# Optimization experiments

Hardware: AMD Instinct MI355X
Metric: run time of the kernel (lower is better)

The kernel has to match this reference:

```python
import jax, jax.numpy as jnp
import numpy as np

L, H, P = 16384, 512, 512
DT_MIN, DT_MAX = 1e-3, 1e-1


def setup_inputs() -> dict:
    key = jax.random.key(0)
    ks = jax.random.split(key, 9)
    u = jax.random.normal(ks[0], (L, H), dtype=jnp.float32)
    # stable diagonal state matrix: Re(Lambda) < 0 (HiPPO-style init)
    Lambda_re = -(0.5 * jax.random.uniform(ks[1], (P,), dtype=jnp.float32) + 1e-3)
    Lambda_im = jnp.pi * jax.random.normal(ks[2], (P,), dtype=jnp.float32)
    # lecun-normal-ish scaling for B (fan-in H) and C (fan-in P)
    B_re = jax.random.normal(ks[3], (P, H), dtype=jnp.float32) / jnp.sqrt(2.0 * H)
    B_im = jax.random.normal(ks[4], (P, H), dtype=jnp.float32) / jnp.sqrt(2.0 * H)
    C_re = jax.random.normal(ks[5], (H, P), dtype=jnp.float32) / jnp.sqrt(2.0 * P)
    C_im = jax.random.normal(ks[6], (H, P), dtype=jnp.float32) / jnp.sqrt(2.0 * P)
    D = jax.random.uniform(ks[7], (H,), dtype=jnp.float32)
    # init_log_steps: uniform in [log(dt_min), log(dt_max)]
    lo, hi = np.log(DT_MIN), np.log(DT_MAX)
    log_step = jax.random.uniform(ks[8], (P,), dtype=jnp.float32, minval=lo, maxval=hi)
    return {"u": u, "Lambda_re": Lambda_re, "Lambda_im": Lambda_im,
            "B_re": B_re, "B_im": B_im, "C_re": C_re, "C_im": C_im,
            "D": D, "log_step": log_step}


def _binary_op(q_i, q_j):
    # associative combine for diagonal linear recurrence (elementwise over (L, P))
    A_i, b_i = q_i
    A_j, b_j = q_j
    return (A_j * A_i, A_j * b_i + b_j)


def reference(u, Lambda_re, Lambda_im, B_re, B_im, C_re, C_im, D, log_step):
    Lambda = Lambda_re + 1j * Lambda_im            # (P,) complex64
    B_tilde = B_re + 1j * B_im                     # (P, H)
    C_tilde = C_re + 1j * C_im                     # (H, P)
    step = jnp.exp(log_step)                       # (P,)
    # zero-order-hold discretization
    Lambda_bar = jnp.exp(Lambda * step)            # (P,)
    B_bar = ((Lambda_bar - 1.0) / Lambda)[:, None] * B_tilde  # (P, H)
    # Bu_t = B_bar @ u_t for all t, as one GEMM: (L, H) @ (H, P)
    Bu = u.astype(B_bar.dtype) @ B_bar.T           # (L, P) complex
    Lambda_el = jnp.broadcast_to(Lambda_bar, Bu.shape)  # (L, P)
    _, xs = jax.lax.associative_scan(_binary_op, (Lambda_el, Bu))  # xs: (L, P)
    # y_t = Re(C_tilde @ x_t) + D * u_t, batched as one GEMM
    ys = (xs @ C_tilde.T).real + D * u             # (L, H)
    return ys.astype(jnp.float32)
```

## Files before the change

### kernel.cpp

```cpp
#include <hip/hip_runtime.h>
#include <stdint.h>

#define L_DIM 16384
#define H_DIM 512
#define P_DIM 512
#define T_CH  32
#define NC    (L_DIM / T_CH)
#define LP    ((size_t)L_DIM * P_DIM)
#define LH    ((size_t)L_DIM * H_DIM)

typedef unsigned short u16;
typedef __attribute__((ext_vector_type(8))) _Float16 f16x8;
typedef __attribute__((ext_vector_type(4))) float f32x4;
typedef __attribute__((ext_vector_type(8))) unsigned short u16x8;

__device__ __forceinline__ u16 f2h(float x) {
    _Float16 h = (_Float16)x;
    return __builtin_bit_cast(u16, h);
}
__device__ __forceinline__ float h2f(u16 h) {
    return (float)__builtin_bit_cast(_Float16, h);
}

__device__ __forceinline__ void gload16(const void* g, void* lds) {
    __builtin_amdgcn_global_load_lds(
        (const __attribute__((address_space(1))) void*)g,
        (__attribute__((address_space(3))) void*)(uintptr_t)lds,
        16, 0, 0);
}

__device__ __forceinline__ f32x4 mfma_f16(f16x8 a, f16x8 b, f32x4 c) {
    return __builtin_amdgcn_mfma_f32_16x16x32_f16(a, b, c, 0, 0, 0);
}

__global__ __launch_bounds__(P_DIM) void prep_kernel(
    const float* __restrict__ Lre, const float* __restrict__ Lim,
    const float* __restrict__ log_step,
    float* __restrict__ lbr, float* __restrict__ lbi,
    float* __restrict__ gre, float* __restrict__ gim,
    float* __restrict__ powr, float* __restrict__ powi)
{
    int p = threadIdx.x;
    float st = expf(log_step[p]);
    float ar = Lre[p] * st, ai = Lim[p] * st;
    float er = expf(ar);
    float lr = er * cosf(ai), li = er * sinf(ai);
    lbr[p] = lr; lbi[p] = li;
    float den = Lre[p] * Lre[p] + Lim[p] * Lim[p];
    float x = lr - 1.0f, y = li;
    gre[p] = (x * Lre[p] + y * Lim[p]) / den;
    gim[p] = (y * Lre[p] - x * Lim[p]) / den;
    float pr = 1.f, pi2 = 0.f;
    powr[p] = 1.f; powi[p] = 0.f;
    for (int k = 1; k <= T_CH; ++k) {
        float nr = pr * lr - pi2 * li;
        float ni = pr * li + pi2 * lr;
        pr = nr; pi2 = ni;
        powr[(size_t)k * P_DIM + p] = pr;
        powi[(size_t)k * P_DIM + p] = pi2;
    }
}

__global__ __launch_bounds__(256) void convert_u(
    const float* __restrict__ u, u16* __restrict__ uh)
{
    size_t i = ((size_t)blockIdx.x * 256 + threadIdx.x) * 8;
    float4 v0 = *(const float4*)(u + i);
    float4 v1 = *(const float4*)(u + i + 4);
    u16x8 h;
    h[0] = f2h(v0.x); h[1] = f2h(v0.y); h[2] = f2h(v0.z); h[3] = f2h(v0.w);
    h[4] = f2h(v1.x); h[5] = f2h(v1.y); h[6] = f2h(v1.z); h[7] = f2h(v1.w);
    *(u16x8*)(uh + i) = h;
}

__global__ __launch_bounds__(256) void build_bcat(
    const float* __restrict__ Bre, const float* __restrict__ Bim,
    const float* __restrict__ gre, const float* __restrict__ gim,
    u16* __restrict__ Bcat)
{
    int idx = blockIdx.x * 256 + threadIdx.x;
    int p = idx >> 9, h = idx & 511;
    float br = Bre[idx], bi = Bim[idx];
    float gr = gre[p], gi = gim[p];
    Bcat[(size_t)p * 512 + h]         = f2h(gr * br - gi * bi);
    Bcat[(size_t)(512 + p) * 512 + h] = f2h(gr * bi + gi * br);
}

__global__ __launch_bounds__(256) void build_ccat(
    const float* __restrict__ Cre, const float* __restrict__ Cim,
    u16* __restrict__ Ccat)
{
    int idx = blockIdx.x * 256 + threadIdx.x;
    int h = idx >> 9, p = idx & 511;
    size_t row = (size_t)h * 1024;
    Ccat[row + p]       = f2h(Cre[idx]);
    Ccat[row + 512 + p] = f2h(-Cim[idx]);
}

template<int KTOT, int NBN, int MODE>
__global__ __launch_bounds__(256, 2) void gemm_mfma(
    const u16* __restrict__ A0, const u16* __restrict__ A1,
    const u16* __restrict__ Bmat,
    void* __restrict__ O0v, void* __restrict__ O1v,
    const float* __restrict__ Dvec, const u16* __restrict__ uIn,
    const float* __restrict__ powr, const float* __restrict__ powi,
    float* __restrict__ Rwr, float* __restrict__ Rwi,
    float* __restrict__ Iwr, float* __restrict__ Iwi)
{
    __shared__ u16 Als[128 * 64];
    __shared__ u16 Bls[128 * 64];

    const u16* Aseg[2] = {A0, A1};

    int b = blockIdx.x;
    int m = (b & 7) * 16 + b / (8 * NBN);
    int n = (b >> 3) & (NBN - 1);
    int m0 = m * 128, n0 = n * 128;

    int tid = threadIdx.x;
    int w = tid >> 6, lane = tid & 63;
    int wm = w >> 1, wn = w & 1;

    f32x4 acc[4][4];
    #pragma unroll
    for (int i = 0; i < 4; ++i)
        #pragma unroll
        for (int j = 0; j < 4; ++j) acc[i][j] = (f32x4)0.f;

    int lr8  = lane >> 3;
    int slin = lane & 7;

    char* AlsB = (char*)&Als[0];
    char* BlsB = (char*)&Bls[0];

    const int NSEG = KTOT / 512;
    #pragma unroll
    for (int seg = 0; seg < NSEG; ++seg) {
        const u16* Ap = Aseg[seg];
        for (int k8 = 0; k8 < 8; ++k8) {
            int ko = k8 * 64;
            int kB = seg * 512 + ko;

            __syncthreads();
            #pragma unroll
            for (int c = 0; c < 4; ++c) {
                int sidx = w * 4 + c;
                int r = sidx * 8 + lr8;
                int g = slin ^ (r & 7);
                const u16* ga = Ap + (size_t)(m0 + r) * 512 + ko + g * 8;
                gload16(ga, AlsB + sidx * 1024);
                const u16* gb = Bmat + (size_t)(n0 + r) * KTOT + kB + g * 8;
                gload16(gb, BlsB + sidx * 1024);
            }
            asm volatile("s_waitcnt vmcnt(0)" ::: "memory");
            __syncthreads();

            f16x8 a[4][2], bf[4][2];
            #pragma unroll
            for (int mm = 0; mm < 4; ++mm)
                #pragma unroll
                for (int kk = 0; kk < 2; ++kk) {
                    int row = wm * 64 + mm * 16 + (lane & 15);
                    int sl  = kk * 4 + (lane >> 4);
                    int off = row * 128 + ((sl ^ (lane & 7)) << 4);
                    a[mm][kk] = *(const f16x8*)(AlsB + off);
                }
            #pragma unroll
            for (int nn = 0; nn < 4; ++nn)
                #pragma unroll
                for (int kk = 0; kk < 2; ++kk) {
                    int row = wn * 64 + nn * 16 + (lane & 15);
                    int sl  = kk * 4 + (lane >> 4);
                    int off = row * 128 + ((sl ^ (lane & 7)) << 4);
                    bf[nn][kk] = *(const f16x8*)(BlsB + off);
                }
            #pragma unroll
            for (int mm = 0; mm < 4; ++mm)
                #pragma unroll
                for (int nn = 0; nn < 4; ++nn) {
                    acc[mm][nn] = mfma_f16(a[mm][0], bf[nn][0], acc[mm][nn]);
                    acc[mm][nn] = mfma_f16(a[mm][1], bf[nn][1], acc[mm][nn]);
                }
        }
    }

    int colb = n0 + wn * 64;
    int rowb = m0 + wm * 64;
    #pragma unroll
    for (int mm = 0; mm < 4; ++mm)
        #pragma unroll
        for (int nn = 0; nn < 4; ++nn) {
            f32x4 v = acc[mm][nn];
            int col = colb + nn * 16 + (lane & 15);
            #pragma unroll
            for (int j = 0; j < 4; ++j) {
                int row = rowb + mm * 16 + (lane >> 4) * 4 + j;
                if constexpr (MODE == 0) {
                    size_t oidx = (size_t)row * 512 + (col & 511);
                    u16 hv = f2h(v[j]);
                    if (col < 512) ((u16*)O0v)[oidx] = hv;
                    else           ((u16*)O1v)[oidx] = hv;
                } else {
                    size_t oidx = (size_t)row * 512 + col;
                    ((float*)O0v)[oidx] = v[j] + Dvec[col] * h2f(uIn[oidx]);
                }
            }
        }

    if constexpr (MODE == 0) {
        float swr[2][4] = {{0.f}};
        float swi[2][4] = {{0.f}};
        #pragma unroll
        for (int mm = 0; mm < 4; ++mm) {
            int ch = mm >> 1;
            #pragma unroll
            for (int nn = 0; nn < 4; ++nn) {
                int col = colb + nn * 16 + (lane & 15);
                int p = col & 511;
                f32x4 v = acc[mm][nn];
                #pragma unroll
                for (int j = 0; j < 4; ++j) {
                    int k = (mm & 1) * 16 + (lane >> 4) * 4 + j;
                    int e = (T_CH - 1) - k;
                    float wr = powr[(size_t)e * 512 + p];
                    float wi = powi[(size_t)e * 512 + p];
                    swr[ch][nn] = fmaf(wr, v[j], swr[ch][nn]);
                    swi[ch][nn] = fmaf(wi, v[j], swi[ch][nn]);
                }
            }
        }
        #pragma unroll
        for (int ch = 0; ch < 2; ++ch)
            #pragma unroll
            for (int nn = 0; nn < 4; ++nn) {
                float a2 = swr[ch][nn];
                a2 += __shfl_xor(a2, 16); a2 += __shfl_xor(a2, 32);
                swr[ch][nn] = a2;
                float b2 = swi[ch][nn];
                b2 += __shfl_xor(b2, 16); b2 += __shfl_xor(b2, 32);
                swi[ch][nn] = b2;
            }
        if (lane < 16) {
            #pragma unroll
            for (int ch = 0; ch < 2; ++ch) {
                int c = (m0 >> 5) + wm * 2 + ch;
                #pragma unroll
                for (int nn = 0; nn < 4; ++nn) {
                    int col = colb + nn * 16 + lane;
                    int p = col & 511;
                    size_t pidx = (size_t)c * 512 + p;
                    if (col < 512) { Rwr[pidx] = swr[ch][nn]; Rwi[pidx] = swi[ch][nn]; }
                    else           { Iwr[pidx] = swr[ch][nn]; Iwi[pidx] = swi[ch][nn]; }
                }
            }
        }
    }
}

__global__ __launch_bounds__(64) void scan_chunks(
    const float* __restrict__ Rwr, const float* __restrict__ Rwi,
    const float* __restrict__ Iwr, const float* __restrict__ Iwi,
    const float* __restrict__ powr, const float* __restrict__ powi,
    float* __restrict__ carr, float* __restrict__ cari)
{
    int p = blockIdx.x * 64 + threadIdx.x;
    float ar = powr[(size_t)T_CH * P_DIM + p];
    float ai = powi[(size_t)T_CH * P_DIM + p];
    float sr = 0.f, si = 0.f;
    #pragma unroll 8
    for (int c = 0; c < NC; ++c) {
        size_t idx = (size_t)c * P_DIM + p;
        carr[idx] = sr; cari[idx] = si;
        float vre = Rwr[idx] - Iwi[idx];
        float vim = Rwi[idx] + Iwr[idx];
        float nr = fmaf(ar, sr, fmaf(-ai, si, vre));
        float ni = fmaf(ar, si, fmaf( ai, sr, vim));
        sr = nr; si = ni;
    }
}

__global__ __launch_bounds__(P_DIM) void scan_fix(
    const u16* __restrict__ burh, const u16* __restrict__ buih,
    const float* __restrict__ lbr, const float* __restrict__ lbi,
    const float* __restrict__ carr, const float* __restrict__ cari,
    u16* __restrict__ xrh, u16* __restrict__ xih)
{
    int p = threadIdx.x;
    int c = blockIdx.x;
    float lr = lbr[p], li = lbi[p];
    float xr = carr[(size_t)c * P_DIM + p];
    float xi = cari[(size_t)c * P_DIM + p];
    size_t base = (size_t)c * T_CH * P_DIM + p;
    #pragma unroll 4
    for (int k = 0; k < T_CH; ++k) {
        size_t idx = base + (size_t)k * P_DIM;
        float br = h2f(burh[idx]), bi = h2f(buih[idx]);
        float nr = fmaf(lr, xr, fmaf(-li, xi, br));
        float ni = fmaf(lr, xi, fmaf( li, xr, bi));
        xr = nr; xi = ni;
        xrh[idx] = f2h(xr);
        xih[idx] = f2h(xi);
    }
}

extern "C" void kernel_launch(void* const* d_in, const int* in_sizes, int n_in,
                              void* d_out, int out_size, void* d_ws, size_t ws_size,
                              hipStream_t stream)
{
    const float* u        = (const float*)d_in[0];
    const float* Lre      = (const float*)d_in[1];
    const float* Lim      = (const float*)d_in[2];
    const float* Bre      = (const float*)d_in[3];
    const float* Bim      = (const float*)d_in[4];
    const float* Cre      = (const float*)d_in[5];
    const float* Cim      = (const float*)d_in[6];
    const float* D        = (const float*)d_in[7];
    const float* log_step = (const float*)d_in[8];
    float* out = (float*)d_out;

    char* w8 = (char*)d_ws;
    u16*   burh = (u16*)(w8);
    u16*   buih = (u16*)(w8 + 16777216);
    u16*   xrh  = (u16*)(w8 + 33554432);
    u16*   xih  = (u16*)(w8 + 50331648);
    u16*   uh   = (u16*)(w8 + 67108864);
    u16*   Bcat = (u16*)(w8 + 83886080);
    u16*   Ccat = (u16*)(w8 + 84934656);
    float* Rwr  = (float*)(w8 + 85983232);
    float* Rwi  = (float*)(w8 + 87031808);
    float* Iwr  = (float*)(w8 + 88080384);
    float* Iwi  = (float*)(w8 + 89128960);
    float* carr = (float*)(w8 + 90177536);
    float* cari = (float*)(w8 + 91226112);
    float* powr = (float*)(w8 + 92274688);
    float* powi = (float*)(w8 + 92342272);
    float* lbr  = (float*)(w8 + 92409856);
    float* lbi  = lbr + P_DIM;
    float* gre  = lbi + P_DIM;
    float* gim  = gre + P_DIM;

    prep_kernel<<<1, P_DIM, 0, stream>>>(Lre, Lim, log_step, lbr, lbi, gre, gim, powr, powi);
    convert_u<<<(int)(LH / 2048), 256, 0, stream>>>(u, uh);
    build_bcat<<<(P_DIM * H_DIM) / 256, 256, 0, stream>>>(Bre, Bim, gre, gim, Bcat);
    build_ccat<<<(H_DIM * P_DIM) / 256, 256, 0, stream>>>(Cre, Cim, Ccat);

    gemm_mfma<512, 8, 0><<<1024, 256, 0, stream>>>(
        uh, uh, Bcat, burh, buih, nullptr, nullptr,
        powr, powi, Rwr, Rwi, Iwr, Iwi);

    scan_chunks<<<8, 64, 0, stream>>>(Rwr, Rwi, Iwr, Iwi, powr, powi, carr, cari);
    scan_fix<<<NC, P_DIM, 0, stream>>>(burh, buih, lbr, lbi, carr, cari, xrh, xih);

    gemm_mfma<1024, 4, 1><<<512, 256, 0, stream>>>(
        xrh, xih, Ccat, out, nullptr, D, uh,
        nullptr, nullptr, nullptr, nullptr, nullptr, nullptr);
}
```

Baseline: 130.6 us.

## Fuse prep, conversion, and B/C build kernels into one front kernel

Merges the four small setup kernels (lambda discretisation and powers, u-to-half conversion, B and C concatenation) into a single launch that partitions blocks by role. The B build now recomputes the ZOH gain per element instead of reading it from a buffer written by a serialized one-block prep kernel. This removes launch overhead and the dependency chain between prep and B build. It also reorders the chunk-weight reduction in the first GEMM epilogue so each power value loaded is reused for both chunk halves.

```diff
diff --git a/kernel.cpp b/kernel.cpp
--- a/kernel.cpp
+++ b/kernel.cpp
@@ -33,68 +33,72 @@
     return __builtin_amdgcn_mfma_f32_16x16x32_f16(a, b, c, 0, 0, 0);
 }
 
-__global__ __launch_bounds__(P_DIM) void prep_kernel(
-    const float* __restrict__ Lre, const float* __restrict__ Lim,
-    const float* __restrict__ log_step,
-    float* __restrict__ lbr, float* __restrict__ lbi,
-    float* __restrict__ gre, float* __restrict__ gim,
-    float* __restrict__ powr, float* __restrict__ powi)
-{
-    int p = threadIdx.x;
+__device__ __forceinline__ void zoh_lambda(
+    const float* Lre, const float* Lim, const float* log_step, int p,
+    float& lr, float& li)
+{
     float st = expf(log_step[p]);
     float ar = Lre[p] * st, ai = Lim[p] * st;
     float er = expf(ar);
-    float lr = er * cosf(ai), li = er * sinf(ai);
-    lbr[p] = lr; lbi[p] = li;
-    float den = Lre[p] * Lre[p] + Lim[p] * Lim[p];
-    float x = lr - 1.0f, y = li;
-    gre[p] = (x * Lre[p] + y * Lim[p]) / den;
-    gim[p] = (y * Lre[p] - x * Lim[p]) / den;
-    float pr = 1.f, pi2 = 0.f;
-    powr[p] = 1.f; powi[p] = 0.f;
-    for (int k = 1; k <= T_CH; ++k) {
-        float nr = pr * lr - pi2 * li;
-        float ni = pr * li + pi2 * lr;
-        pr = nr; pi2 = ni;
-        powr[(size_t)k * P_DIM + p] = pr;
-        powi[(size_t)k * P_DIM + p] = pi2;
-    }
-}
-
-__global__ __launch_bounds__(256) void convert_u(
-    const float* __restrict__ u, u16* __restrict__ uh)
-{
-    size_t i = ((size_t)blockIdx.x * 256 + threadIdx.x) * 8;
-    float4 v0 = *(const float4*)(u + i);
-    float4 v1 = *(const float4*)(u + i + 4);
-    u16x8 h;
-    h[0] = f2h(v0.x); h[1] = f2h(v0.y); h[2] = f2h(v0.z); h[3] = f2h(v0.w);
-    h[4] = f2h(v1.x); h[5] = f2h(v1.y); h[6] = f2h(v1.z); h[7] = f2h(v1.w);
-    *(u16x8*)(uh + i) = h;
-}
-
-__global__ __launch_bounds__(256) void build_bcat(
+    lr = er * cosf(ai);
+    li = er * sinf(ai);
+}
+
+__global__ __launch_bounds__(256) void front_kernel(
+    const float* __restrict__ u,
+    const float* __restrict__ Lre, const float* __restrict__ Lim,
+    const float* __restrict__ log_step,
     const float* __restrict__ Bre, const float* __restrict__ Bim,
-    const float* __restrict__ gre, const float* __restrict__ gim,
-    u16* __restrict__ Bcat)
-{
-    int idx = blockIdx.x * 256 + threadIdx.x;
-    int p = idx >> 9, h = idx & 511;
-    float br = Bre[idx], bi = Bim[idx];
-    float gr = gre[p], gi = gim[p];
-    Bcat[(size_t)p * 512 + h]         = f2h(gr * br - gi * bi);
-    Bcat[(size_t)(512 + p) * 512 + h] = f2h(gr * bi + gi * br);
-}
-
-__global__ __launch_bounds__(256) void build_ccat(
     const float* __restrict__ Cre, const float* __restrict__ Cim,
-    u16* __restrict__ Ccat)
-{
-    int idx = blockIdx.x * 256 + threadIdx.x;
-    int h = idx >> 9, p = idx & 511;
-    size_t row = (size_t)h * 1024;
-    Ccat[row + p]       = f2h(Cre[idx]);
-    Ccat[row + 512 + p] = f2h(-Cim[idx]);
+    u16* __restrict__ uh, u16* __restrict__ Bcat, u16* __restrict__ Ccat,
+    float* __restrict__ lbr, float* __restrict__ lbi,
+    float* __restrict__ powr, float* __restrict__ powi)
+{
+    int b = blockIdx.x;
+    if (b < 4096) {
+        size_t i = ((size_t)b * 256 + threadIdx.x) * 8;
+        float4 v0 = *(const float4*)(u + i);
+        float4 v1 = *(const float4*)(u + i + 4);
+        u16x8 h;
+        h[0] = f2h(v0.x); h[1] = f2h(v0.y); h[2] = f2h(v0.z); h[3] = f2h(v0.w);
+        h[4] = f2h(v1.x); h[5] = f2h(v1.y); h[6] = f2h(v1.z); h[7] = f2h(v1.w);
+        *(u16x8*)(uh + i) = h;
+    } else if (b < 5120) {
+        int idx = (b - 4096) * 256 + threadIdx.x;
+        int p = idx >> 9, h = idx & 511;
+        float lr, li;
+        zoh_lambda(Lre, Lim, log_step, p, lr, li);
+        float den = Lre[p] * Lre[p] + Lim[p] * Lim[p];
+        float x = lr - 1.0f, y = li;
+        float gr = (x * Lre[p] + y * Lim[p]) / den;
+        float gi = (y * Lre[p] - x * Lim[p]) / den;
+        float br = Bre[idx], bi = Bim[idx];
+        Bcat[(size_t)p * 512 + h]         = f2h(gr * br - gi * bi);
+        Bcat[(size_t)(512 + p) * 512 + h] = f2h(gr * bi + gi * br);
+    } else if (b < 6144) {
+        int idx = (b - 5120) * 256 + threadIdx.x;
+        int h = idx >> 9, p = idx & 511;
+        size_t row = (size_t)h * 1024;
+        Ccat[row + p]       = f2h(Cre[idx]);
+        Ccat[row + 512 + p] = f2h(-Cim[idx]);
+    } else {
+        #pragma unroll
+        for (int t = 0; t < 2; ++t) {
+            int p = threadIdx.x + t * 256;
+            float lr, li;
+            zoh_lambda(Lre, Lim, log_step, p, lr, li);
+            lbr[p] = lr; lbi[p] = li;
+            float pr = 1.f, pi2 = 0.f;
+            powr[p] = 1.f; powi[p] = 0.f;
+            for (int k = 1; k <= T_CH; ++k) {
+                float nr = pr * lr - pi2 * li;
+                float ni = pr * li + pi2 * lr;
+                pr = nr; pi2 = ni;
+                powr[(size_t)k * P_DIM + p] = pr;
+                powi[(size_t)k * P_DIM + p] = pi2;
+            }
+        }
+    }
 }
 
 template<int KTOT, int NBN, int MODE>
@@ -211,24 +215,22 @@
         float swr[2][4] = {{0.f}};
         float swi[2][4] = {{0.f}};
         #pragma unroll
-        for (int mm = 0; mm < 4; ++mm) {
-            int ch = mm >> 1;
-            #pragma unroll
-            for (int nn = 0; nn < 4; ++nn) {
-                int col = colb + nn * 16 + (lane & 15);
-                int p = col & 511;
-                f32x4 v = acc[mm][nn];
-                #pragma unroll
-                for (int j = 0; j < 4; ++j) {
-                    int k = (mm & 1) * 16 + (lane >> 4) * 4 + j;
-                    int e = (T_CH - 1) - k;
+        for (int h = 0; h < 2; ++h)
+            #pragma unroll
+            for (int j = 0; j < 4; ++j) {
+                int k = h * 16 + (lane >> 4) * 4 + j;
+                int e = (T_CH - 1) - k;
+                #pragma unroll
+                for (int nn = 0; nn < 4; ++nn) {
+                    int p = (colb + nn * 16 + (lane & 15)) & 511;
                     float wr = powr[(size_t)e * 512 + p];
                     float wi = powi[(size_t)e * 512 + p];
-                    swr[ch][nn] = fmaf(wr, v[j], swr[ch][nn]);
-                    swi[ch][nn] = fmaf(wi, v[j], swi[ch][nn]);
-                }
-            }
-        }
+                    swr[0][nn] = fmaf(wr, acc[h][nn][j],     swr[0][nn]);
+                    swi[0][nn] = fmaf(wi, acc[h][nn][j],     swi[0][nn]);
+                    swr[1][nn] = fmaf(wr, acc[2 + h][nn][j], swr[1][nn]);
+                    swi[1][nn] = fmaf(wi, acc[2 + h][nn][j], swi[1][nn]);
+                }
+            }
         #pragma unroll
         for (int ch = 0; ch < 2; ++ch)
             #pragma unroll
@@ -336,13 +338,10 @@
     float* powi = (float*)(w8 + 92342272);
     float* lbr  = (float*)(w8 + 92409856);
     float* lbi  = lbr + P_DIM;
-    float* gre  = lbi + P_DIM;
-    float* gim  = gre + P_DIM;
-
-    prep_kernel<<<1, P_DIM, 0, stream>>>(Lre, Lim, log_step, lbr, lbi, gre, gim, powr, powi);
-    convert_u<<<(int)(LH / 2048), 256, 0, stream>>>(u, uh);
-    build_bcat<<<(P_DIM * H_DIM) / 256, 256, 0, stream>>>(Bre, Bim, gre, gim, Bcat);
-    build_ccat<<<(H_DIM * P_DIM) / 256, 256, 0, stream>>>(Cre, Cim, Ccat);
+
+    front_kernel<<<6145, 256, 0, stream>>>(
+        u, Lre, Lim, log_step, Bre, Bim, Cre, Cim,
+        uh, Bcat, Ccat, lbr, lbi, powr, powi);
 
     gemm_mfma<512, 8, 0><<<1024, 256, 0, stream>>>(
         uh, uh, Bcat, burh, buih, nullptr, nullptr,
```

Result: faster. 121.9 us (-6.7%).
